# Kernel optimization log

Hardware: AMD Instinct MI355X
Metric: run time of the kernel (lower is better)

Reference implementation:

```python
import jax, jax.numpy as jnp
import numpy as np

D = 16          # manifold_dim
M = 8192        # mem_slots
H = 256         # slot_dim
K_BASE = 32     # topk
K_BIG = 48      # int(K_BASE * 1.5), used when internal lightbulb fires
INPUT_DIM = 1024
ODE_HID = 128
ODE_STEPS = 2
ODE_DT = 0.5
TEMPERATURE = 1.0      # buffer initial value
LB_TOP1_AVG = 1.0      # buffer initial value
LB_DROP_RATIO = 0.7
BIG = 1e30


def layer_norm(x, g, b, eps=1e-5):
    mu = jnp.mean(x, axis=-1, keepdims=True)
    var = jnp.mean(jnp.square(x - mu), axis=-1, keepdims=True)
    return (x - mu) * jax.lax.rsqrt(var + eps) * g + b


def setup_inputs() -> dict:
    key = jax.random.key(0)
    ks = jax.random.split(key, 12)
    B, S = 4, 2048
    T3 = D * 3
    s_in = 1.0 / np.sqrt(INPUT_DIM)
    s_3d = 1.0 / np.sqrt(T3)
    s_h = 1.0 / np.sqrt(H)
    s_ode = 1.0 / np.sqrt(ODE_HID)
    return {
        "x": jax.random.normal(ks[0], (B, S, INPUT_DIM), jnp.float32),
        "W_proj": jax.random.normal(ks[1], (INPUT_DIM, T3), jnp.float32) * s_in,
        "b_proj": jnp.zeros((T3,), jnp.float32),
        "ln1_g": jnp.ones((T3,), jnp.float32),
        "ln1_b": jnp.zeros((T3,), jnp.float32),
        "ode_W1": jax.random.normal(ks[2], (T3, ODE_HID), jnp.float32) * s_3d,
        "ode_b1": jnp.zeros((ODE_HID,), jnp.float32),
        "ode_W2": jax.random.normal(ks[3], (ODE_HID, T3), jnp.float32) * s_ode,
        "ode_b2": jnp.zeros((T3,), jnp.float32),
        "memory_slots": jax.random.normal(ks[4], (M, H), jnp.float32),
        "pos_enc": jax.random.normal(ks[5], (M, D, 3), jnp.float32),
        "curvature": jax.random.normal(ks[6], (M, D), jnp.float32),
        "curv_alpha": jnp.float32(0.1),
        "W_out": jax.random.normal(ks[7], (H, INPUT_DIM), jnp.float32) * s_h,
        "b_out": jnp.zeros((INPUT_DIM,), jnp.float32),
        "ln2_g": jnp.ones((INPUT_DIM,), jnp.float32),
        "ln2_b": jnp.zeros((INPUT_DIM,), jnp.float32),
    }


def reference(x, W_proj, b_proj, ln1_g, ln1_b, ode_W1, ode_b1, ode_W2, ode_b2,
              memory_slots, pos_enc, curvature, curv_alpha, W_out, b_out, ln2_g, ln2_b):
    # manifold projection: Linear -> LayerNorm -> GELU   (B,S,3D)
    h = jax.nn.gelu(layer_norm(x @ W_proj + b_proj, ln1_g, ln1_b), approximate=False)
    # ODE evolution (2 steps): x + dt * MLP(x), operating on flattened (B,S,3D)
    for _ in range(ODE_STEPS):
        dh = jnp.tanh(h @ ode_W1 + ode_b1) @ ode_W2 + ode_b2
        h = h + ODE_DT * dh
    # _attend: query positions are detached in the original
    q = jax.lax.stop_gradient(h)                       # (B,S,3D)
    mem_pos = pos_enc.reshape(M, D * 3)                # (M,3D)
    # fast pairwise squared-L2 distance: ||q||^2 + ||m||^2 - 2 q.m
    q2 = jnp.sum(q * q, axis=-1, keepdims=True)        # (B,S,1)
    m2 = jnp.sum(mem_pos * mem_pos, axis=-1)           # (M,)
    dist = jnp.maximum(q2 + m2 - 2.0 * jnp.einsum('bsd,md->bsm', q, mem_pos), 0.0)
    dist = dist / max(TEMPERATURE, 1e-6)
    curv_w = jnp.exp(-curv_alpha * jnp.linalg.norm(curvature, axis=-1))  # (M,)
    dist = dist * curv_w                               # (B,S,M)
    # dynamic top-K: take K_BIG smallest, mask down to K_BASE if lightbulb not fired
    neg_vals, itop = jax.lax.top_k(-dist, K_BIG)       # smallest K_BIG distances
    dtop = -neg_vals                                    # ascending (B,S,K_BIG)
    top1 = jnp.mean(dtop[..., 0])
    internal_fire = top1 < LB_DROP_RATIO * LB_TOP1_AVG
    keep = jnp.logical_or(internal_fire, jnp.arange(K_BIG) < K_BASE)  # (K_BIG,)
    d_eff = jnp.where(keep, dtop, BIG)
    w = jax.nn.softmax(-d_eff, axis=-1)                # (B,S,K_BIG)
    mem = memory_slots[itop]                           # gather (B,S,K_BIG,H)
    attended = jnp.einsum('bsk,bskh->bsh', w, mem)     # (B,S,H)
    out = jax.nn.gelu(layer_norm(attended @ W_out + b_out, ln2_g, ln2_b), approximate=False)
    return out
```

## Files before the change

### kernel.cpp

```cpp
#include <hip/hip_runtime.h>
#include <math.h>

#define NQ    8192
#define T3    48
#define INDIM 1024
#define HID   128
#define MSLOT 8192
#define HD    256
#define KBIG  48
#define KBASE 32
#define CHUNK 4096

#define OFF_QH    ((size_t)0)
#define OFF_QL    ((size_t)1048576)
#define OFF_Q2    ((size_t)2097152)
#define OFF_M2    ((size_t)2129920)
#define OFF_CW    ((size_t)2162688)
#define OFF_TOPV  ((size_t)2195456)
#define OFF_TOPI  ((size_t)3768320)
#define OFF_RMIN  ((size_t)5341184)
#define OFF_FLAG  ((size_t)5373952)
#define OFF_WOT   ((size_t)5374208)
#define OFF_PEH   ((size_t)5898496)
#define OFF_PEL   ((size_t)6947072)
#define OFF_WPTH  ((size_t)7995648)
#define OFF_WPTL  ((size_t)8093952)
#define OFF_H0    ((size_t)8192256)
#define OFF_BIG   ((size_t)9765120)

typedef __attribute__((ext_vector_type(8))) short short8;
typedef __attribute__((ext_vector_type(4))) float f32x4;

__device__ __forceinline__ float gelu_exact(float x) {
    return 0.5f * x * (1.0f + erff(x * 0.70710678118654752f));
}

__device__ __forceinline__ unsigned short bf16_rne(float f) {
    unsigned int x = __float_as_uint(f);
    unsigned int r = (x + 0x7fffu + ((x >> 16) & 1u)) >> 16;
    return (unsigned short)r;
}

__device__ __forceinline__ void split2(float x, unsigned short& h, unsigned short& l) {
    h = bf16_rne(x);
    l = bf16_rne(x - __uint_as_float((unsigned)h << 16));
}

__global__ __launch_bounds__(256) void k0_prep(const float* __restrict__ pe,
        const float* __restrict__ curv, const float* __restrict__ alpha,
        float* __restrict__ m2, float* __restrict__ cw,
        unsigned short* __restrict__ ph, unsigned short* __restrict__ pl) {
    int m = blockIdx.x * 256 + threadIdx.x;
    float s = 0.f;
    for (int d = 0; d < T3; d++) { float v = pe[(size_t)m * T3 + d]; s += v * v; }
    m2[m] = s;
    float c = 0.f;
    for (int d = 0; d < 16; d++) { float v = curv[m * 16 + d]; c += v * v; }
    cw[m] = expf(-alpha[0] * sqrtf(c));
    int base = blockIdx.x * 256;
    for (int idx = threadIdx.x; idx < 256 * 64; idx += 256) {
        int r = idx >> 6, cc = idx & 63;
        unsigned short hi = 0, lo = 0;
        if (cc < T3) split2(pe[(size_t)(base + r) * T3 + cc], hi, lo);
        size_t o = (size_t)(base + r) * 64 + cc;
        ph[o] = hi; pl[o] = lo;
    }
}

__global__ __launch_bounds__(256) void k0b_cvt(const float* __restrict__ Wo,
        unsigned short* __restrict__ Wot) {
    __shared__ float t[64][65];
    int k0 = blockIdx.x * 64;
    int n0 = blockIdx.y * 64;
    int c = threadIdx.x & 63, r4 = threadIdx.x >> 6;
    #pragma unroll
    for (int i = 0; i < 16; i++) {
        int kr = i * 4 + r4;
        t[kr][c] = Wo[(size_t)(k0 + kr) * INDIM + n0 + c];
    }
    __syncthreads();
    #pragma unroll
    for (int i = 0; i < 16; i++) {
        int nr = i * 4 + r4;
        Wot[(size_t)(n0 + nr) * HD + k0 + c] = bf16_rne(t[c][nr]);
    }
}

__global__ __launch_bounds__(256) void k0c_xsplit(const float* __restrict__ x,
        unsigned short* __restrict__ xh, unsigned short* __restrict__ xl) {
    size_t base = ((size_t)blockIdx.x * 256 + threadIdx.x) * 8;
    float4 a = *(const float4*)(x + base);
    float4 b = *(const float4*)(x + base + 4);
    unsigned short h[8], l[8];
    split2(a.x, h[0], l[0]); split2(a.y, h[1], l[1]);
    split2(a.z, h[2], l[2]); split2(a.w, h[3], l[3]);
    split2(b.x, h[4], l[4]); split2(b.y, h[5], l[5]);
    split2(b.z, h[6], l[6]); split2(b.w, h[7], l[7]);
    uint4 hv, lv;
    hv.x = h[0] | ((unsigned)h[1] << 16); hv.y = h[2] | ((unsigned)h[3] << 16);
    hv.z = h[4] | ((unsigned)h[5] << 16); hv.w = h[6] | ((unsigned)h[7] << 16);
    lv.x = l[0] | ((unsigned)l[1] << 16); lv.y = l[2] | ((unsigned)l[3] << 16);
    lv.z = l[4] | ((unsigned)l[5] << 16); lv.w = l[6] | ((unsigned)l[7] << 16);
    *(uint4*)(xh + base) = hv;
    *(uint4*)(xl + base) = lv;
}

__global__ __launch_bounds__(256) void k0d_wpt(const float* __restrict__ Wp,
        unsigned short* __restrict__ wph, unsigned short* __restrict__ wpl) {
    int n = blockIdx.x;
    for (int k = threadIdx.x; k < INDIM; k += 256) {
        unsigned short h, l;
        split2(Wp[(size_t)k * T3 + n], h, l);
        wph[(size_t)n * INDIM + k] = h;
        wpl[(size_t)n * INDIM + k] = l;
    }
}

__global__ __launch_bounds__(256) void k1_mfma(const unsigned short* __restrict__ xh,
        const unsigned short* __restrict__ xl,
        const unsigned short* __restrict__ wph, const unsigned short* __restrict__ wpl,
        float* __restrict__ h0) {
    __shared__ float part[4][32][48];
    int tid = threadIdx.x, lane = tid & 63, wv = tid >> 6;
    int r0 = blockIdx.x * 32;
    int lm = lane & 15, lk8 = (lane >> 4) * 8;
    f32x4 acc[2][3];
    #pragma unroll
    for (int i = 0; i < 2; i++)
        #pragma unroll
        for (int j = 0; j < 3; j++) acc[i][j] = (f32x4)(0.f);
    int kw = wv * 256;
    #pragma unroll 2
    for (int ks = 0; ks < 8; ks++) {
        int kofs = kw + ks * 32 + lk8;
        short8 ah[2], al[2], bh[3], bl[3];
        #pragma unroll
        for (int i = 0; i < 2; i++) {
            size_t ao = (size_t)(r0 + i * 16 + lm) * INDIM + kofs;
            ah[i] = *(const short8*)(xh + ao);
            al[i] = *(const short8*)(xl + ao);
        }
        #pragma unroll
        for (int j = 0; j < 3; j++) {
            size_t bo = (size_t)(j * 16 + lm) * INDIM + kofs;
            bh[j] = *(const short8*)(wph + bo);
            bl[j] = *(const short8*)(wpl + bo);
        }
        #pragma unroll
        for (int i = 0; i < 2; i++)
            #pragma unroll
            for (int j = 0; j < 3; j++) {
                f32x4 a = acc[i][j];
                a = __builtin_amdgcn_mfma_f32_16x16x32_bf16(ah[i], bh[j], a, 0, 0, 0);
                a = __builtin_amdgcn_mfma_f32_16x16x32_bf16(ah[i], bl[j], a, 0, 0, 0);
                a = __builtin_amdgcn_mfma_f32_16x16x32_bf16(al[i], bh[j], a, 0, 0, 0);
                acc[i][j] = a;
            }
    }
    int orow = (lane >> 4) * 4;
    #pragma unroll
    for (int i = 0; i < 2; i++)
        #pragma unroll
        for (int j = 0; j < 3; j++)
            #pragma unroll
            for (int r = 0; r < 4; r++)
                part[wv][i * 16 + orow + r][j * 16 + lm] = acc[i][j][r];
    __syncthreads();
    for (int idx = tid; idx < 32 * 48; idx += 256) {
        int rr = idx / 48, cc = idx - rr * 48;
        float s = part[0][rr][cc] + part[1][rr][cc] + part[2][rr][cc] + part[3][rr][cc];
        h0[(size_t)(r0 + rr) * T3 + cc] = s;
    }
}

__global__ __launch_bounds__(256) void k1b_ode(const float* __restrict__ h0,
        const float* __restrict__ bp,
        const float* __restrict__ g1, const float* __restrict__ b1ln,
        const float* __restrict__ W1, const float* __restrict__ bb1,
        const float* __restrict__ W2, const float* __restrict__ bb2,
        unsigned short* __restrict__ qh, unsigned short* __restrict__ ql,
        float* __restrict__ q2out) {
    __shared__ __align__(16) float W1s[T3 * HID];
    __shared__ __align__(16) float W2s[HID * T3];
    __shared__ __align__(16) float hs[16 * T3];
    __shared__ __align__(16) float t1s[16 * 132];
    int tid = threadIdx.x;
    size_t base = (size_t)blockIdx.x * 16 * T3;
    for (int i = tid; i < 1536; i += 256) {
        *(float4*)&W1s[i * 4] = *(const float4*)&W1[i * 4];
        *(float4*)&W2s[i * 4] = *(const float4*)&W2[i * 4];
    }
    for (int idx = tid; idx < 16 * T3; idx += 256) {
        int c = idx % T3;
        t1s[idx] = bp[c] + h0[base + idx];
    }
    __syncthreads();
    {
        int r = tid >> 4, c16 = tid & 15;
        float v[3];
        float ssum = 0.f;
        #pragma unroll
        for (int i = 0; i < 3; i++) { v[i] = t1s[r * T3 + c16 * 3 + i]; ssum += v[i]; }
        #pragma unroll
        for (int off = 1; off < 16; off <<= 1) ssum += __shfl_xor(ssum, off);
        float mean = ssum * (1.f / T3);
        float vv = 0.f;
        #pragma unroll
        for (int i = 0; i < 3; i++) { v[i] -= mean; vv += v[i] * v[i]; }
        #pragma unroll
        for (int off = 1; off < 16; off <<= 1) vv += __shfl_xor(vv, off);
        float rstd = rsqrtf(vv * (1.f / T3) + 1e-5f);
        #pragma unroll
        for (int i = 0; i < 3; i++) {
            int c = c16 * 3 + i;
            hs[r * T3 + c] = gelu_exact(v[i] * rstd * g1[c] + b1ln[c]);
        }
    }
    __syncthreads();
    for (int step = 0; step < 2; step++) {
        #pragma unroll
        for (int it = 0; it < 2; it++) {
            int idx = tid + it * 256;
            int rr = idx >> 5, j4 = idx & 31;
            float4 a = *(const float4*)&bb1[j4 * 4];
            #pragma unroll 3
            for (int d4 = 0; d4 < 12; d4++) {
                float4 qv = *(const float4*)&hs[rr * T3 + d4 * 4];
                float qa[4] = {qv.x, qv.y, qv.z, qv.w};
                #pragma unroll
                for (int dd = 0; dd < 4; dd++) {
                    float4 wv = *(const float4*)&W1s[(d4 * 4 + dd) * HID + j4 * 4];
                    a.x += qa[dd] * wv.x; a.y += qa[dd] * wv.y;
                    a.z += qa[dd] * wv.z; a.w += qa[dd] * wv.w;
                }
            }
            a.x = tanhf(a.x); a.y = tanhf(a.y); a.z = tanhf(a.z); a.w = tanhf(a.w);
            *(float4*)&t1s[rr * 132 + j4 * 4] = a;
        }
        __syncthreads();
        if (tid < 192) {
            int rr = tid / 12, c4 = tid % 12;
            float4 a = *(const float4*)&bb2[c4 * 4];
            #pragma unroll 4
            for (int j4 = 0; j4 < 32; j4++) {
                float4 tv = *(const float4*)&t1s[rr * 132 + j4 * 4];
                float ta[4] = {tv.x, tv.y, tv.z, tv.w};
                #pragma unroll
                for (int jj = 0; jj < 4; jj++) {
                    float4 wv = *(const float4*)&W2s[(j4 * 4 + jj) * T3 + c4 * 4];
                    a.x += ta[jj] * wv.x; a.y += ta[jj] * wv.y;
                    a.z += ta[jj] * wv.z; a.w += ta[jj] * wv.w;
                }
            }
            float4 cur = *(const float4*)&hs[rr * T3 + c4 * 4];
            cur.x += 0.5f * a.x; cur.y += 0.5f * a.y;
            cur.z += 0.5f * a.z; cur.w += 0.5f * a.w;
            *(float4*)&hs[rr * T3 + c4 * 4] = cur;
        }
        __syncthreads();
    }
    {
        int r = tid >> 4, c16 = tid & 15;
        float sq = 0.f;
        #pragma unroll
        for (int i = 0; i < 3; i++) { float v = hs[r * T3 + c16 * 3 + i]; sq += v * v; }
        #pragma unroll
        for (int off = 1; off < 16; off <<= 1) sq += __shfl_xor(sq, off);
        if (c16 == 0) q2out[(size_t)blockIdx.x * 16 + r] = sq;
    }
    for (int idx = tid; idx < 16 * 64; idx += 256) {
        int r = idx >> 6, c = idx & 63;
        unsigned short hi = 0, lo = 0;
        if (c < T3) split2(hs[r * T3 + c], hi, lo);
        size_t o = ((size_t)blockIdx.x * 16 + r) * 64 + c;
        qh[o] = hi; ql[o] = lo;
    }
}

#define PES 72
__global__ __launch_bounds__(256) void k2a_mfma(
        const unsigned short* __restrict__ qh, const unsigned short* __restrict__ ql,
        const float* __restrict__ q2g,
        const unsigned short* __restrict__ ph, const unsigned short* __restrict__ pl,
        const float* __restrict__ m2, const float* __restrict__ cw,
        float* __restrict__ dist, int rowbase) {
    __shared__ __align__(16) char smem[2 * 256 * PES * 2];
    __shared__ float q2s[64];
    unsigned short* pesh = (unsigned short*)smem;
    unsigned short* pesl = (unsigned short*)smem + 256 * PES;
    int tid = threadIdx.x, lane = tid & 63, wv = tid >> 6;
    int c0 = blockIdx.x * 256;
    int r0 = blockIdx.y * 64;
    int grow0 = rowbase + r0;
    for (int idx = tid; idx < 2048; idx += 256) {
        int col = idx >> 3, ch = idx & 7;
        *(uint4*)&pesh[col * PES + ch * 8] = *(const uint4*)&ph[(size_t)(c0 + col) * 64 + ch * 8];
        *(uint4*)&pesl[col * PES + ch * 8] = *(const uint4*)&pl[(size_t)(c0 + col) * 64 + ch * 8];
    }
    if (tid < 64) q2s[tid] = q2g[grow0 + tid];
    int lm = lane & 15, lk8 = (lane >> 4) * 8;
    short8 bqh[4][2], bql[4][2];
    #pragma unroll
    for (int qs = 0; qs < 4; qs++)
        #pragma unroll
        for (int ks = 0; ks < 2; ks++) {
            size_t o = (size_t)(grow0 + qs * 16 + lm) * 64 + ks * 32 + lk8;
            bqh[qs][ks] = *(const short8*)&qh[o];
            bql[qs][ks] = *(const short8*)&ql[o];
        }
    __syncthreads();
    f32x4 acc[4][4];
    #pragma unroll
    for (int i = 0; i < 4; i++)
        #pragma unroll
        for (int j = 0; j < 4; j++) acc[i][j] = (f32x4)(0.f);
    int mco = wv * 64;
    #pragma unroll
    for (int ms = 0; ms < 4; ms++) {
        int arow = mco + ms * 16 + lm;
        short8 ah0 = *(const short8*)&pesh[arow * PES + lk8];
        short8 ah1 = *(const short8*)&pesh[arow * PES + 32 + lk8];
        short8 al0 = *(const short8*)&pesl[arow * PES + lk8];
        short8 al1 = *(const short8*)&pesl[arow * PES + 32 + lk8];
        #pragma unroll
        for (int qs = 0; qs < 4; qs++) {
            f32x4 a = acc[ms][qs];
            a = __builtin_amdgcn_mfma_f32_16x16x32_bf16(ah0, bqh[qs][0], a, 0, 0, 0);
            a = __builtin_amdgcn_mfma_f32_16x16x32_bf16(ah1, bqh[qs][1], a, 0, 0, 0);
            a = __builtin_amdgcn_mfma_f32_16x16x32_bf16(ah0, bql[qs][0], a, 0, 0, 0);
            a = __builtin_amdgcn_mfma_f32_16x16x32_bf16(ah1, bql[qs][1], a, 0, 0, 0);
            a = __builtin_amdgcn_mfma_f32_16x16x32_bf16(al0, bqh[qs][0], a, 0, 0, 0);
            a = __builtin_amdgcn_mfma_f32_16x16x32_bf16(al1, bqh[qs][1], a, 0, 0, 0);
            acc[ms][qs] = a;
        }
    }
    int mr4 = (lane >> 4) * 4;
    float4 ov[4][4];
    #pragma unroll
    for (int ms = 0; ms < 4; ms++) {
        int gm = c0 + mco + ms * 16 + mr4;
        float4 m2v = *(const float4*)&m2[gm];
        float4 cwv = *(const float4*)&cw[gm];
        #pragma unroll
        for (int qs = 0; qs < 4; qs++) {
            float q2 = q2s[qs * 16 + lm];
            f32x4 a = acc[ms][qs];
            float4 o;
            o.x = fmaxf(q2 + m2v.x - 2.f * a[0], 0.f) * cwv.x;
            o.y = fmaxf(q2 + m2v.y - 2.f * a[1], 0.f) * cwv.y;
            o.z = fmaxf(q2 + m2v.z - 2.f * a[2], 0.f) * cwv.z;
            o.w = fmaxf(q2 + m2v.w - 2.f * a[3], 0.f) * cwv.w;
            ov[ms][qs] = o;
        }
    }
    __syncthreads();
    float (*dt)[260] = (float(*)[260])smem;
    #pragma unroll
    for (int ms = 0; ms < 4; ms++)
        #pragma unroll
        for (int qs = 0; qs < 4; qs++)
            *(float4*)&dt[qs * 16 + lm][mco + ms * 16 + mr4] = ov[ms][qs];
    __syncthreads();
    #pragma unroll
    for (int i = 0; i < 16; i++) {
        int qrow = wv * 16 + i;
        float4 v = *(const float4*)&dt[qrow][lane * 4];
        *(float4*)&dist[(size_t)(r0 + qrow) * MSLOT + c0 + lane * 4] = v;
    }
}

#define NBIN2 2048
#define MAXCAND 1024
__global__ __launch_bounds__(256) void k2b_topk(const float* __restrict__ dist,
        float* __restrict__ topv, int* __restrict__ topi,
        float* __restrict__ rowmin, int rowbase) {
    __shared__ unsigned int hist[NBIN2];
    __shared__ unsigned long long cand[MAXCAND];
    __shared__ float s_wmin[4], s_wmax[4];
    __shared__ unsigned int wsum[4];
    __shared__ unsigned int s_B, s_ncand;
    int tid = threadIdx.x, lane = tid & 63, wv = tid >> 6;
    int rl = blockIdx.x;
    size_t row = (size_t)(rowbase + rl);
    const float4* src = (const float4*)(dist + (size_t)rl * MSLOT);
    float fv[32];
    #pragma unroll
    for (int j = 0; j < 8; j++) {
        float4 v = src[tid + 256 * j];
        fv[j * 4 + 0] = v.x; fv[j * 4 + 1] = v.y;
        fv[j * 4 + 2] = v.z; fv[j * 4 + 3] = v.w;
    }
    float mn = fv[0], mx = fv[0];
    #pragma unroll
    for (int j = 1; j < 32; j++) { mn = fminf(mn, fv[j]); mx = fmaxf(mx, fv[j]); }
    #pragma unroll
    for (int off = 32; off; off >>= 1) {
        mn = fminf(mn, __shfl_xor(mn, off));
        mx = fmaxf(mx, __shfl_xor(mx, off));
    }
    if (lane == 0) { s_wmin[wv] = mn; s_wmax[wv] = mx; }
    __syncthreads();
    float m0 = fminf(fminf(s_wmin[0], s_wmin[1]), fminf(s_wmin[2], s_wmin[3]));
    float mX = fmaxf(fmaxf(s_wmax[0], s_wmax[1]), fmaxf(s_wmax[2], s_wmax[3]));
    float lo = m0;
    float width = fmaxf(m0 * 0.5f, 1e-3f);
    float fullw = fmaxf((mX - m0) * 1.0001f, 1e-3f) + 1e-6f;
    unsigned B = 0;
    float scale = 0.f, hiT = 0.f;
    for (int att = 0; att < 7; att++) {
        if (att == 6 || width > fullw) width = fullw;
        hiT = lo + width;
        scale = (float)NBIN2 / width;
        for (int i = tid; i < NBIN2; i += 256) hist[i] = 0;
        __syncthreads();
        #pragma unroll
        for (int j = 0; j < 32; j++) {
            float v = fv[j];
            if (v < hiT) {
                int b = (int)((v - lo) * scale);
                b = b < NBIN2 - 1 ? b : NBIN2 - 1;
                atomicAdd(&hist[b], 1u);
            }
        }
        __syncthreads();
        unsigned hb[8];
        unsigned s = 0;
        #pragma unroll
        for (int i = 0; i < 8; i++) { hb[i] = hist[tid * 8 + i]; s += hb[i]; }
        unsigned v = s;
        #pragma unroll
        for (int off = 1; off < 64; off <<= 1) {
            unsigned o = __shfl_up(v, off);
            if (lane >= off) v += o;
        }
        if (lane == 63) wsum[wv] = v;
        __syncthreads();
        unsigned wbase = 0;
        for (int w = 0; w < wv; w++) wbase += wsum[w];
        unsigned total = wsum[0] + wsum[1] + wsum[2] + wsum[3];
        if (total >= KBIG) {
            unsigned excl = wbase + v - s;
            if (excl < KBIG && KBIG <= excl + s) {
                unsigned c = excl;
                #pragma unroll
                for (int i = 0; i < 8; i++) {
                    if (c < KBIG && KBIG <= c + hb[i]) { s_B = tid * 8 + i; break; }
                    c += hb[i];
                }
            }
            __syncthreads();
            B = s_B;
            break;
        }
        width *= 8.f;
        __syncthreads();
    }
    if (tid == 0) s_ncand = 0;
    __syncthreads();
    #pragma unroll
    for (int j = 0; j < 32; j++) {
        float v = fv[j];
        if (v < hiT) {
            int b = (int)((v - lo) * scale);
            b = b < NBIN2 - 1 ? b : NBIN2 - 1;
            if ((unsigned)b <= B) {
                unsigned n = atomicAdd(&s_ncand, 1u);
                if (n < MAXCAND) {
                    int m = ((tid + 256 * (j >> 2)) << 2) + (j & 3);
                    cand[n] = ((unsigned long long)__float_as_uint(v) << 32) | (unsigned)m;
                }
            }
        }
    }
    __syncthreads();
    int nc = (int)(s_ncand < MAXCAND ? s_ncand : MAXCAND);
    for (int i = tid; i < nc; i += 256) {
        unsigned long long me = cand[i];
        int rank = 0;
        for (int j = 0; j < nc; j++) rank += (cand[j] < me) ? 1 : 0;
        if (rank < KBIG) {
            float v = __uint_as_float((unsigned)(me >> 32));
            topv[row * KBIG + rank] = v;
            topi[row * KBIG + rank] = (int)(me & 0xFFFFFFFFu);
            if (rank == 0) rowmin[row] = v;
        }
    }
}

__global__ __launch_bounds__(256) void k3a_flag(const float* __restrict__ rowmin,
        int* __restrict__ flag) {
    __shared__ float red[256];
    int tid = threadIdx.x;
    float s = 0.f;
    for (int j = 0; j < NQ / 256; j++) s += rowmin[tid + 256 * j];
    red[tid] = s;
    __syncthreads();
    for (int st = 128; st; st >>= 1) {
        if (tid < st) red[tid] += red[tid + st];
        __syncthreads();
    }
    if (tid == 0) {
        float top1 = red[0] / (float)NQ;
        flag[0] = (top1 < 0.7f) ? 1 : 0;
    }
}

__global__ __launch_bounds__(256) void k3_attend(const float* __restrict__ topv,
        const int* __restrict__ topi, const int* __restrict__ flag,
        const float* __restrict__ slots, unsigned short* __restrict__ attb) {
    int tid = threadIdx.x;
    int lane = tid & 63, wv = tid >> 6;
    size_t row = (size_t)blockIdx.x * 4 + wv;
    int kc = flag[0] ? KBIG : KBASE;
    float v0 = topv[row * KBIG];
    float ev = 0.f;
    int mi = 0;
    if (lane < KBIG) {
        float v = topv[row * KBIG + lane];
        ev = (lane < kc) ? expf(-(v - v0)) : 0.f;
        mi = topi[row * KBIG + lane];
    }
    float ssum = ev;
    #pragma unroll
    for (int off = 32; off; off >>= 1) ssum += __shfl_xor(ssum, off);
    float inv = 1.f / ssum;
    float4 acc = make_float4(0.f, 0.f, 0.f, 0.f);
    for (int k = 0; k < kc; k++) {
        float wk = __shfl(ev, k) * inv;
        int m = __shfl(mi, k);
        float4 v = *(const float4*)(slots + (size_t)m * HD + lane * 4);
        acc.x += wk * v.x; acc.y += wk * v.y;
        acc.z += wk * v.z; acc.w += wk * v.w;
    }
    ushort4 o;
    o.x = bf16_rne(acc.x); o.y = bf16_rne(acc.y);
    o.z = bf16_rne(acc.z); o.w = bf16_rne(acc.w);
    *(ushort4*)(attb + row * HD + lane * 4) = o;
}

__global__ __launch_bounds__(256) void k4_mfma(const unsigned short* __restrict__ A,
        const unsigned short* __restrict__ Bt, const float* __restrict__ bo,
        float* __restrict__ out) {
    int tid = threadIdx.x;
    int lane = tid & 63, wave = tid >> 6;
    int wm = wave >> 1, wn = wave & 1;
    int mbase = blockIdx.y * 128 + wm * 64;
    int nbase = blockIdx.x * 128 + wn * 64;
    int lm = lane & 15;
    int lk8 = (lane >> 4) * 8;
    f32x4 acc[4][4];
    #pragma unroll
    for (int i = 0; i < 4; i++)
        #pragma unroll
        for (int j = 0; j < 4; j++) acc[i][j] = (f32x4)(0.f);
    #pragma unroll 2
    for (int ks = 0; ks < 8; ks++) {
        int kofs = ks * 32 + lk8;
        short8 a[4], b[4];
        #pragma unroll
        for (int i = 0; i < 4; i++)
            a[i] = *(const short8*)(A + (size_t)(mbase + i * 16 + lm) * HD + kofs);
        #pragma unroll
        for (int j = 0; j < 4; j++)
            b[j] = *(const short8*)(Bt + (size_t)(nbase + j * 16 + lm) * HD + kofs);
        #pragma unroll
        for (int i = 0; i < 4; i++)
            #pragma unroll
            for (int j = 0; j < 4; j++)
                acc[i][j] = __builtin_amdgcn_mfma_f32_16x16x32_bf16(a[i], b[j], acc[i][j], 0, 0, 0);
    }
    int orow = (lane >> 4) * 4;
    #pragma unroll
    for (int i = 0; i < 4; i++)
        #pragma unroll
        for (int j = 0; j < 4; j++) {
            int col = nbase + j * 16 + lm;
            float bias = bo[col];
            #pragma unroll
            for (int r = 0; r < 4; r++) {
                int row = mbase + i * 16 + orow + r;
                out[(size_t)row * INDIM + col] = acc[i][j][r] + bias;
            }
        }
}

__global__ __launch_bounds__(256) void k5_ln(float* __restrict__ out,
        const float* __restrict__ g, const float* __restrict__ b) {
    __shared__ float red[4];
    int tid = threadIdx.x;
    size_t row = blockIdx.x;
    float4 v = *(const float4*)(out + row * INDIM + tid * 4);
    float s = v.x + v.y + v.z + v.w;
    #pragma unroll
    for (int off = 32; off; off >>= 1) s += __shfl_xor(s, off);
    int wid = tid >> 6, lane = tid & 63;
    if (!lane) red[wid] = s;
    __syncthreads();
    float mean = (red[0] + red[1] + red[2] + red[3]) * (1.f / (float)INDIM);
    __syncthreads();
    float dx = v.x - mean, dy = v.y - mean, dz = v.z - mean, dw = v.w - mean;
    float ss = dx * dx + dy * dy + dz * dz + dw * dw;
    #pragma unroll
    for (int off = 32; off; off >>= 1) ss += __shfl_xor(ss, off);
    if (!lane) red[wid] = ss;
    __syncthreads();
    float var = (red[0] + red[1] + red[2] + red[3]) * (1.f / (float)INDIM);
    float rs = rsqrtf(var + 1e-5f);
    int c = tid * 4;
    float4 o;
    o.x = gelu_exact(dx * rs * g[c + 0] + b[c + 0]);
    o.y = gelu_exact(dy * rs * g[c + 1] + b[c + 1]);
    o.z = gelu_exact(dz * rs * g[c + 2] + b[c + 2]);
    o.w = gelu_exact(dw * rs * g[c + 3] + b[c + 3]);
    *(float4*)(out + row * INDIM + c) = o;
}

extern "C" void kernel_launch(void* const* d_in, const int* in_sizes, int n_in,
                              void* d_out, int out_size, void* d_ws, size_t ws_size,
                              hipStream_t stream) {
    const float* x     = (const float*)d_in[0];
    const float* Wp    = (const float*)d_in[1];
    const float* bp    = (const float*)d_in[2];
    const float* ln1g  = (const float*)d_in[3];
    const float* ln1b  = (const float*)d_in[4];
    const float* oW1   = (const float*)d_in[5];
    const float* ob1   = (const float*)d_in[6];
    const float* oW2   = (const float*)d_in[7];
    const float* ob2   = (const float*)d_in[8];
    const float* slots = (const float*)d_in[9];
    const float* pe    = (const float*)d_in[10];
    const float* curv  = (const float*)d_in[11];
    const float* alpha = (const float*)d_in[12];
    const float* Wo    = (const float*)d_in[13];
    const float* bo    = (const float*)d_in[14];
    const float* ln2g  = (const float*)d_in[15];
    const float* ln2b  = (const float*)d_in[16];
    float* out = (float*)d_out;
    char* ws = (char*)d_ws;

    unsigned short* qhp = (unsigned short*)(ws + OFF_QH);
    unsigned short* qlp = (unsigned short*)(ws + OFF_QL);
    float* q2p    = (float*)(ws + OFF_Q2);
    float* m2     = (float*)(ws + OFF_M2);
    float* cwv    = (float*)(ws + OFF_CW);
    float* topv   = (float*)(ws + OFF_TOPV);
    int*   topi   = (int*)  (ws + OFF_TOPI);
    float* rowmin = (float*)(ws + OFF_RMIN);
    int*   flag   = (int*)  (ws + OFF_FLAG);
    unsigned short* wot  = (unsigned short*)(ws + OFF_WOT);
    unsigned short* peh  = (unsigned short*)(ws + OFF_PEH);
    unsigned short* pel  = (unsigned short*)(ws + OFF_PEL);
    unsigned short* wpth = (unsigned short*)(ws + OFF_WPTH);
    unsigned short* wptl = (unsigned short*)(ws + OFF_WPTL);
    float* h0     = (float*)(ws + OFF_H0);
    unsigned short* xh = (unsigned short*)(ws + OFF_BIG);
    unsigned short* xl = (unsigned short*)(ws + OFF_BIG + (size_t)16777216);
    float* dist   = (float*)(ws + OFF_BIG);
    unsigned short* attb = (unsigned short*)(ws + OFF_BIG);

    k0_prep<<<MSLOT / 256, 256, 0, stream>>>(pe, curv, alpha, m2, cwv, peh, pel);
    k0b_cvt<<<dim3(4, 16), 256, 0, stream>>>(Wo, wot);
    k0c_xsplit<<<(NQ * INDIM) / 2048, 256, 0, stream>>>(x, xh, xl);
    k0d_wpt<<<T3, 256, 0, stream>>>(Wp, wpth, wptl);
    k1_mfma<<<NQ / 32, 256, 0, stream>>>(xh, xl, wpth, wptl, h0);
    k1b_ode<<<NQ / 16, 256, 0, stream>>>(h0, bp, ln1g, ln1b, oW1, ob1, oW2, ob2,
                                         qhp, qlp, q2p);
    for (int ch = 0; ch < NQ / CHUNK; ch++) {
        k2a_mfma<<<dim3(MSLOT / 256, CHUNK / 64), 256, 0, stream>>>(
            qhp, qlp, q2p, peh, pel, m2, cwv, dist, ch * CHUNK);
        k2b_topk<<<CHUNK, 256, 0, stream>>>(dist, topv, topi, rowmin, ch * CHUNK);
    }
    k3a_flag<<<1, 256, 0, stream>>>(rowmin, flag);
    k3_attend<<<NQ / 4, 256, 0, stream>>>(topv, topi, flag, slots, attb);
    k4_mfma<<<dim3(INDIM / 128, NQ / 128), 256, 0, stream>>>(attb, wot, bo, out);
    k5_ln<<<NQ, 256, 0, stream>>>(out, ln2g, ln2b);
}
```

Baseline: 296.4 us.

## Replace full distance matrix top-k with sampled-threshold filter and candidate select

Instead of writing the full 8192x8192 distance matrix and running a histogram top-k per row, distances against the first 1024 slots are computed to get a per-row 48th-smallest threshold. The distance GEMM is then recomputed over all slots, and only values at or below the threshold are appended via atomics to a per-row candidate list, which a final kernel ranks exactly. Separately, the x hi/lo bf16 split is fused into the projection GEMM, removing the xsplit kernel and its intermediate buffers. The filter avoids the large dist write and read, at the cost of per-candidate global atomics and a CAP of 1024 candidates per row that could overflow.

```diff
diff --git a/kernel.cpp b/kernel.cpp
--- a/kernel.cpp
+++ b/kernel.cpp
@@ -9,7 +9,8 @@
 #define HD    256
 #define KBIG  48
 #define KBASE 32
-#define CHUNK 4096
+#define NSAMP 1024
+#define CAP   1024
 
 #define OFF_QH    ((size_t)0)
 #define OFF_QL    ((size_t)1048576)
@@ -26,7 +27,11 @@
 #define OFF_WPTH  ((size_t)7995648)
 #define OFF_WPTL  ((size_t)8093952)
 #define OFF_H0    ((size_t)8192256)
-#define OFF_BIG   ((size_t)9765120)
+#define OFF_RTHR  ((size_t)9765120)
+#define OFF_CNT   ((size_t)9797888)
+#define OFF_ATTB  ((size_t)9830656)
+#define OFF_DISTS ((size_t)14024960)
+#define OFF_CANDS ((size_t)47579392)
 
 typedef __attribute__((ext_vector_type(8))) short short8;
 typedef __attribute__((ext_vector_type(4))) float f32x4;
@@ -86,25 +91,6 @@
     }
 }
 
-__global__ __launch_bounds__(256) void k0c_xsplit(const float* __restrict__ x,
-        unsigned short* __restrict__ xh, unsigned short* __restrict__ xl) {
-    size_t base = ((size_t)blockIdx.x * 256 + threadIdx.x) * 8;
-    float4 a = *(const float4*)(x + base);
-    float4 b = *(const float4*)(x + base + 4);
-    unsigned short h[8], l[8];
-    split2(a.x, h[0], l[0]); split2(a.y, h[1], l[1]);
-    split2(a.z, h[2], l[2]); split2(a.w, h[3], l[3]);
-    split2(b.x, h[4], l[4]); split2(b.y, h[5], l[5]);
-    split2(b.z, h[6], l[6]); split2(b.w, h[7], l[7]);
-    uint4 hv, lv;
-    hv.x = h[0] | ((unsigned)h[1] << 16); hv.y = h[2] | ((unsigned)h[3] << 16);
-    hv.z = h[4] | ((unsigned)h[5] << 16); hv.w = h[6] | ((unsigned)h[7] << 16);
-    lv.x = l[0] | ((unsigned)l[1] << 16); lv.y = l[2] | ((unsigned)l[3] << 16);
-    lv.z = l[4] | ((unsigned)l[5] << 16); lv.w = l[6] | ((unsigned)l[7] << 16);
-    *(uint4*)(xh + base) = hv;
-    *(uint4*)(xl + base) = lv;
-}
-
 __global__ __launch_bounds__(256) void k0d_wpt(const float* __restrict__ Wp,
         unsigned short* __restrict__ wph, unsigned short* __restrict__ wpl) {
     int n = blockIdx.x;
@@ -116,8 +102,7 @@
     }
 }
 
-__global__ __launch_bounds__(256) void k1_mfma(const unsigned short* __restrict__ xh,
-        const unsigned short* __restrict__ xl,
+__global__ __launch_bounds__(256) void k1_mfma(const float* __restrict__ x,
         const unsigned short* __restrict__ wph, const unsigned short* __restrict__ wpl,
         float* __restrict__ h0) {
     __shared__ float part[4][32][48];
@@ -130,15 +115,21 @@
         #pragma unroll
         for (int j = 0; j < 3; j++) acc[i][j] = (f32x4)(0.f);
     int kw = wv * 256;
-    #pragma unroll 2
     for (int ks = 0; ks < 8; ks++) {
         int kofs = kw + ks * 32 + lk8;
         short8 ah[2], al[2], bh[3], bl[3];
         #pragma unroll
         for (int i = 0; i < 2; i++) {
-            size_t ao = (size_t)(r0 + i * 16 + lm) * INDIM + kofs;
-            ah[i] = *(const short8*)(xh + ao);
-            al[i] = *(const short8*)(xl + ao);
+            const float* xp = x + (size_t)(r0 + i * 16 + lm) * INDIM + kofs;
+            float4 xa = *(const float4*)xp;
+            float4 xb = *(const float4*)(xp + 4);
+            float va[8] = {xa.x, xa.y, xa.z, xa.w, xb.x, xb.y, xb.z, xb.w};
+            #pragma unroll
+            for (int e = 0; e < 8; e++) {
+                unsigned short h, l;
+                split2(va[e], h, l);
+                ah[i][e] = (short)h; al[i][e] = (short)l;
+            }
         }
         #pragma unroll
         for (int j = 0; j < 3; j++) {
@@ -283,15 +274,14 @@
         const float* __restrict__ q2g,
         const unsigned short* __restrict__ ph, const unsigned short* __restrict__ pl,
         const float* __restrict__ m2, const float* __restrict__ cw,
-        float* __restrict__ dist, int rowbase) {
+        float* __restrict__ dist, int rowstride) {
     __shared__ __align__(16) char smem[2 * 256 * PES * 2];
     __shared__ float q2s[64];
     unsigned short* pesh = (unsigned short*)smem;
     unsigned short* pesl = (unsigned short*)smem + 256 * PES;
     int tid = threadIdx.x, lane = tid & 63, wv = tid >> 6;
     int c0 = blockIdx.x * 256;
-    int r0 = blockIdx.y * 64;
-    int grow0 = rowbase + r0;
+    int grow0 = blockIdx.y * 64;
     for (int idx = tid; idx < 2048; idx += 256) {
         int col = idx >> 3, ch = idx & 7;
         *(uint4*)&pesh[col * PES + ch * 8] = *(const uint4*)&ph[(size_t)(c0 + col) * 64 + ch * 8];
@@ -365,34 +355,25 @@
     for (int i = 0; i < 16; i++) {
         int qrow = wv * 16 + i;
         float4 v = *(const float4*)&dt[qrow][lane * 4];
-        *(float4*)&dist[(size_t)(r0 + qrow) * MSLOT + c0 + lane * 4] = v;
-    }
-}
-
-#define NBIN2 2048
-#define MAXCAND 1024
-__global__ __launch_bounds__(256) void k2b_topk(const float* __restrict__ dist,
-        float* __restrict__ topv, int* __restrict__ topi,
-        float* __restrict__ rowmin, int rowbase) {
-    __shared__ unsigned int hist[NBIN2];
-    __shared__ unsigned long long cand[MAXCAND];
+        *(float4*)&dist[(size_t)(grow0 + qrow) * rowstride + c0 + lane * 4] = v;
+    }
+}
+
+#define NBINT 2048
+#define MAXCT 512
+__global__ __launch_bounds__(256) void k2b_thr(const float* __restrict__ dists,
+        float* __restrict__ rowthr, int* __restrict__ cnt) {
+    __shared__ unsigned int hist[NBINT];
+    __shared__ unsigned long long cand[MAXCT];
     __shared__ float s_wmin[4], s_wmax[4];
     __shared__ unsigned int wsum[4];
     __shared__ unsigned int s_B, s_ncand;
     int tid = threadIdx.x, lane = tid & 63, wv = tid >> 6;
-    int rl = blockIdx.x;
-    size_t row = (size_t)(rowbase + rl);
-    const float4* src = (const float4*)(dist + (size_t)rl * MSLOT);
-    float fv[32];
-    #pragma unroll
-    for (int j = 0; j < 8; j++) {
-        float4 v = src[tid + 256 * j];
-        fv[j * 4 + 0] = v.x; fv[j * 4 + 1] = v.y;
-        fv[j * 4 + 2] = v.z; fv[j * 4 + 3] = v.w;
-    }
-    float mn = fv[0], mx = fv[0];
-    #pragma unroll
-    for (int j = 1; j < 32; j++) { mn = fminf(mn, fv[j]); mx = fmaxf(mx, fv[j]); }
+    int row = blockIdx.x;
+    float4 v4 = *(const float4*)(dists + (size_t)row * NSAMP + tid * 4);
+    float fv[4] = {v4.x, v4.y, v4.z, v4.w};
+    float mn = fminf(fminf(fv[0], fv[1]), fminf(fv[2], fv[3]));
+    float mx = fmaxf(fmaxf(fv[0], fv[1]), fmaxf(fv[2], fv[3]));
     #pragma unroll
     for (int off = 32; off; off >>= 1) {
         mn = fminf(mn, __shfl_xor(mn, off));
@@ -410,15 +391,15 @@
     for (int att = 0; att < 7; att++) {
         if (att == 6 || width > fullw) width = fullw;
         hiT = lo + width;
-        scale = (float)NBIN2 / width;
-        for (int i = tid; i < NBIN2; i += 256) hist[i] = 0;
+        scale = (float)NBINT / width;
+        for (int i = tid; i < NBINT; i += 256) hist[i] = 0;
         __syncthreads();
         #pragma unroll
-        for (int j = 0; j < 32; j++) {
+        for (int j = 0; j < 4; j++) {
             float v = fv[j];
             if (v < hiT) {
                 int b = (int)((v - lo) * scale);
-                b = b < NBIN2 - 1 ? b : NBIN2 - 1;
+                b = b < NBINT - 1 ? b : NBINT - 1;
                 atomicAdd(&hist[b], 1u);
             }
         }
@@ -458,26 +439,134 @@
     if (tid == 0) s_ncand = 0;
     __syncthreads();
     #pragma unroll
-    for (int j = 0; j < 32; j++) {
+    for (int j = 0; j < 4; j++) {
         float v = fv[j];
         if (v < hiT) {
             int b = (int)((v - lo) * scale);
-            b = b < NBIN2 - 1 ? b : NBIN2 - 1;
+            b = b < NBINT - 1 ? b : NBINT - 1;
             if ((unsigned)b <= B) {
                 unsigned n = atomicAdd(&s_ncand, 1u);
-                if (n < MAXCAND) {
-                    int m = ((tid + 256 * (j >> 2)) << 2) + (j & 3);
-                    cand[n] = ((unsigned long long)__float_as_uint(v) << 32) | (unsigned)m;
-                }
-            }
-        }
-    }
-    __syncthreads();
-    int nc = (int)(s_ncand < MAXCAND ? s_ncand : MAXCAND);
+                if (n < MAXCT)
+                    cand[n] = ((unsigned long long)__float_as_uint(v) << 32)
+                              | (unsigned)(tid * 4 + j);
+            }
+        }
+    }
+    __syncthreads();
+    int nc = (int)(s_ncand < MAXCT ? s_ncand : MAXCT);
     for (int i = tid; i < nc; i += 256) {
         unsigned long long me = cand[i];
         int rank = 0;
         for (int j = 0; j < nc; j++) rank += (cand[j] < me) ? 1 : 0;
+        if (rank == KBIG - 1)
+            rowthr[row] = __uint_as_float((unsigned)(me >> 32));
+    }
+    if (tid == 0) cnt[row] = 0;
+}
+
+__global__ __launch_bounds__(256) void k2c_filter(
+        const unsigned short* __restrict__ qh, const unsigned short* __restrict__ ql,
+        const float* __restrict__ q2g,
+        const unsigned short* __restrict__ ph, const unsigned short* __restrict__ pl,
+        const float* __restrict__ m2, const float* __restrict__ cw,
+        const float* __restrict__ rowthr, int* __restrict__ cnt,
+        unsigned long long* __restrict__ cands) {
+    __shared__ __align__(16) unsigned short pesh[256 * PES];
+    __shared__ __align__(16) unsigned short pesl[256 * PES];
+    __shared__ float q2s[64];
+    __shared__ float thrs[64];
+    int tid = threadIdx.x, lane = tid & 63, wv = tid >> 6;
+    int c0 = blockIdx.x * 256;
+    int grow0 = blockIdx.y * 64;
+    for (int idx = tid; idx < 2048; idx += 256) {
+        int col = idx >> 3, ch = idx & 7;
+        *(uint4*)&pesh[col * PES + ch * 8] = *(const uint4*)&ph[(size_t)(c0 + col) * 64 + ch * 8];
+        *(uint4*)&pesl[col * PES + ch * 8] = *(const uint4*)&pl[(size_t)(c0 + col) * 64 + ch * 8];
+    }
+    if (tid < 64) {
+        q2s[tid] = q2g[grow0 + tid];
+        thrs[tid] = rowthr[grow0 + tid];
+    }
+    int lm = lane & 15, lk8 = (lane >> 4) * 8;
+    short8 bqh[4][2], bql[4][2];
+    #pragma unroll
+    for (int qs = 0; qs < 4; qs++)
+        #pragma unroll
+        for (int ks = 0; ks < 2; ks++) {
+            size_t o = (size_t)(grow0 + qs * 16 + lm) * 64 + ks * 32 + lk8;
+            bqh[qs][ks] = *(const short8*)&qh[o];
+            bql[qs][ks] = *(const short8*)&ql[o];
+        }
+    __syncthreads();
+    f32x4 acc[4][4];
+    #pragma unroll
+    for (int i = 0; i < 4; i++)
+        #pragma unroll
+        for (int j = 0; j < 4; j++) acc[i][j] = (f32x4)(0.f);
+    int mco = wv * 64;
+    #pragma unroll
+    for (int ms = 0; ms < 4; ms++) {
+        int arow = mco + ms * 16 + lm;
+        short8 ah0 = *(const short8*)&pesh[arow * PES + lk8];
+        short8 ah1 = *(const short8*)&pesh[arow * PES + 32 + lk8];
+        short8 al0 = *(const short8*)&pesl[arow * PES + lk8];
+        short8 al1 = *(const short8*)&pesl[arow * PES + 32 + lk8];
+        #pragma unroll
+        for (int qs = 0; qs < 4; qs++) {
+            f32x4 a = acc[ms][qs];
+            a = __builtin_amdgcn_mfma_f32_16x16x32_bf16(ah0, bqh[qs][0], a, 0, 0, 0);
+            a = __builtin_amdgcn_mfma_f32_16x16x32_bf16(ah1, bqh[qs][1], a, 0, 0, 0);
+            a = __builtin_amdgcn_mfma_f32_16x16x32_bf16(ah0, bql[qs][0], a, 0, 0, 0);
+            a = __builtin_amdgcn_mfma_f32_16x16x32_bf16(ah1, bql[qs][1], a, 0, 0, 0);
+            a = __builtin_amdgcn_mfma_f32_16x16x32_bf16(al0, bqh[qs][0], a, 0, 0, 0);
+            a = __builtin_amdgcn_mfma_f32_16x16x32_bf16(al1, bqh[qs][1], a, 0, 0, 0);
+            acc[ms][qs] = a;
+        }
+    }
+    int mr4 = (lane >> 4) * 4;
+    #pragma unroll
+    for (int ms = 0; ms < 4; ms++) {
+        int gm = c0 + mco + ms * 16 + mr4;
+        float4 m2v = *(const float4*)&m2[gm];
+        float4 cwv = *(const float4*)&cw[gm];
+        float m2a[4] = {m2v.x, m2v.y, m2v.z, m2v.w};
+        float cwa[4] = {cwv.x, cwv.y, cwv.z, cwv.w};
+        #pragma unroll
+        for (int qs = 0; qs < 4; qs++) {
+            int q = qs * 16 + lm;
+            int grow = grow0 + q;
+            float q2 = q2s[q];
+            float thr = thrs[q];
+            f32x4 a = acc[ms][qs];
+            #pragma unroll
+            for (int c = 0; c < 4; c++) {
+                float v = fmaxf(q2 + m2a[c] - 2.f * a[c], 0.f) * cwa[c];
+                if (v <= thr) {
+                    int slot = atomicAdd(&cnt[grow], 1);
+                    if (slot < CAP)
+                        cands[(size_t)grow * CAP + slot] =
+                            ((unsigned long long)__float_as_uint(v) << 32)
+                            | (unsigned)(gm + c);
+                }
+            }
+        }
+    }
+}
+
+__global__ __launch_bounds__(256) void k2d_select(
+        const unsigned long long* __restrict__ cands, const int* __restrict__ cnt,
+        float* __restrict__ topv, int* __restrict__ topi, float* __restrict__ rowmin) {
+    __shared__ unsigned long long cl[CAP];
+    int tid = threadIdx.x;
+    size_t row = blockIdx.x;
+    int nc = cnt[row];
+    nc = nc < CAP ? nc : CAP;
+    for (int i = tid; i < nc; i += 256) cl[i] = cands[row * CAP + i];
+    __syncthreads();
+    for (int i = tid; i < nc; i += 256) {
+        unsigned long long me = cl[i];
+        int rank = 0;
+        for (int j = 0; j < nc; j++) rank += (cl[j] < me) ? 1 : 0;
         if (rank < KBIG) {
             float v = __uint_as_float((unsigned)(me >> 32));
             topv[row * KBIG + rank] = v;
@@ -653,23 +742,24 @@
     unsigned short* wpth = (unsigned short*)(ws + OFF_WPTH);
     unsigned short* wptl = (unsigned short*)(ws + OFF_WPTL);
     float* h0     = (float*)(ws + OFF_H0);
-    unsigned short* xh = (unsigned short*)(ws + OFF_BIG);
-    unsigned short* xl = (unsigned short*)(ws + OFF_BIG + (size_t)16777216);
-    float* dist   = (float*)(ws + OFF_BIG);
-    unsigned short* attb = (unsigned short*)(ws + OFF_BIG);
+    float* rowthr = (float*)(ws + OFF_RTHR);
+    int*   cntp   = (int*)  (ws + OFF_CNT);
+    unsigned short* attb = (unsigned short*)(ws + OFF_ATTB);
+    float* dists  = (float*)(ws + OFF_DISTS);
+    unsigned long long* cands = (unsigned long long*)(ws + OFF_CANDS);
 
     k0_prep<<<MSLOT / 256, 256, 0, stream>>>(pe, curv, alpha, m2, cwv, peh, pel);
     k0b_cvt<<<dim3(4, 16), 256, 0, stream>>>(Wo, wot);
-    k0c_xsplit<<<(NQ * INDIM) / 2048, 256, 0, stream>>>(x, xh, xl);
     k0d_wpt<<<T3, 256, 0, stream>>>(Wp, wpth, wptl);
-    k1_mfma<<<NQ / 32, 256, 0, stream>>>(xh, xl, wpth, wptl, h0);
+    k1_mfma<<<NQ / 32, 256, 0, stream>>>(x, wpth, wptl, h0);
     k1b_ode<<<NQ / 16, 256, 0, stream>>>(h0, bp, ln1g, ln1b, oW1, ob1, oW2, ob2,
                                          qhp, qlp, q2p);
-    for (int ch = 0; ch < NQ / CHUNK; ch++) {
-        k2a_mfma<<<dim3(MSLOT / 256, CHUNK / 64), 256, 0, stream>>>(
-            qhp, qlp, q2p, peh, pel, m2, cwv, dist, ch * CHUNK);
-        k2b_topk<<<CHUNK, 256, 0, stream>>>(dist, topv, topi, rowmin, ch * CHUNK);
-    }
+    k2a_mfma<<<dim3(NSAMP / 256, NQ / 64), 256, 0, stream>>>(
+        qhp, qlp, q2p, peh, pel, m2, cwv, dists, NSAMP);
+    k2b_thr<<<NQ, 256, 0, stream>>>(dists, rowthr, cntp);
+    k2c_filter<<<dim3(MSLOT / 256, NQ / 64), 256, 0, stream>>>(
+        qhp, qlp, q2p, peh, pel, m2, cwv, rowthr, cntp, cands);
+    k2d_select<<<NQ, 256, 0, stream>>>(cands, cntp, topv, topi, rowmin);
     k3a_flag<<<1, 256, 0, stream>>>(rowmin, flag);
     k3_attend<<<NQ / 4, 256, 0, stream>>>(topv, topi, flag, slots, attb);
     k4_mfma<<<dim3(INDIM / 128, NQ / 128), 256, 0, stream>>>(attb, wot, bo, out);
```

Result: slower. 597.3 us (+101.5%).
